# Optimization experiments

Hardware: AMD Instinct MI355X
Metric: run time of the kernel (lower is better)

Reference implementation:

```python
import jax, jax.numpy as jnp
import numpy as np

L = 2
K = 9                      # (L+1)^2 spherical coefficients
N_NODES = 10000
N_EDGES = 80000
C_SPH = 64
C_HID = 64
NHEAD = 8
A_ALPHA = 32
A_VAL = 16
C_OUT = 64
S_GATE = 1 + 2 * L         # gate chunks o_s, o_d^l, o_t^l
EXTRA = NHEAD * A_ALPHA + S_GATE * C_HID   # 256 + 320 = 576

# l-primary -> m-primary permutation for L=2 (m=0 block, then per m: +m coeffs, -m coeffs)
PERM = np.array([0, 2, 6, 3, 7, 1, 5, 8, 4])
INV_PERM = np.argsort(PERM)
L_IDX = np.array([0, 1, 1, 1, 2, 2, 2, 2, 2])  # l of each l-primary coefficient


def scaled_silu(x):
    return jax.nn.silu(x) * (1.0 / 0.6)


def layer_norm(x, w, b, eps=1e-5):
    mu = jnp.mean(x, axis=-1, keepdims=True)
    var = jnp.var(x, axis=-1, keepdims=True)
    return (x - mu) * jax.lax.rsqrt(var + eps) * w + b


def smooth_leaky_relu(x, alpha=0.2):
    return 0.5 * (1 + alpha) * x + 0.5 * (1 - alpha) * x * (2.0 * jax.nn.sigmoid(x) - 1.0)


def _so2_m(x, W):
    # x: [E,2,nin] (row0=+m coeffs, row1=-m coeffs), W: [nin, 2*ncoef*cout]
    y = jnp.einsum('eri,io->ero', x, W)
    half = W.shape[1] // 2
    yr, yi = y[..., :half], y[..., half:]
    out_r = yr[:, 0] - yi[:, 1]
    out_i = yr[:, 1] + yi[:, 0]
    return jnp.stack([out_r, out_i], axis=1)  # [E,2,ncoef*cout]


def so2_conv(emb, cin, cout, wm0, bm0, wm1, wm2, rad=None, extra=0):
    # emb: [E,K,cin] l-primary; block-diagonal per-m SO(2) convolution
    E = emb.shape[0]
    e = emb[:, PERM, :]
    x0 = e[:, 0:3, :].reshape(E, 3 * cin)
    if rad is not None:
        x0 = x0 * rad[:, :3 * cin]
    x0 = x0 @ wm0 + bm0
    x0_extra = None
    if extra:
        x0_extra = x0[:, :extra]
        x0 = x0[:, extra:]
    out0 = x0.reshape(E, 3, cout)
    x1 = e[:, 3:7, :].reshape(E, 2, 2 * cin)
    if rad is not None:
        x1 = x1 * rad[:, 3 * cin:5 * cin][:, None, :]
    out1 = _so2_m(x1, wm1).reshape(E, 4, cout)
    x2 = e[:, 7:9, :].reshape(E, 2, cin)
    if rad is not None:
        x2 = x2 * rad[:, 5 * cin:6 * cin][:, None, :]
    out2 = _so2_m(x2, wm2).reshape(E, 2, cout)
    out = jnp.concatenate([out0, out1, out2], axis=1)[:, INV_PERM, :]
    return out, x0_extra


def _forward(x, atomic_numbers, edge_distance, edge_index, t_ij, rl_ij, wigner, wigner_inv,
             src_emb, tgt_emb, rad_w1, rad_b1, rad_ln_w, rad_ln_b, rad_w2, rad_b2,
             c1_wm0, c1_bm0, c1_wm1, c1_wm2, ln_a_w, ln_a_b, alpha_dot,
             gata_wh, gata_wx, gata_wt, c2_wm0, c2_bm0, c2_wm1, c2_wm2, proj_w, proj_b):
    src, tgt = edge_index[0], edge_index[1]
    x_edge = jnp.concatenate([edge_distance, src_emb[atomic_numbers[src]], tgt_emb[atomic_numbers[tgt]]], axis=1)
    x_src = x[src]                                   # [E,K,C_SPH] gather
    x_tgt = x[tgt]
    h_j = x_tgt[:, 0, :]                              # neighbour scalar part
    X_j = x_tgt[:, 1:, :]                             # neighbour steerable part
    msg = jnp.concatenate([x_src, x_tgt], axis=2)     # [E,K,2*C_SPH]
    msg = jnp.einsum('eij,ejc->eic', wigner, msg)     # per-edge SO(3) rotation
    # radial function: Linear + LayerNorm + ScaledSiLU + Linear
    r = scaled_silu(layer_norm(x_edge @ rad_w1 + rad_b1, rad_ln_w, rad_ln_b)) @ rad_w2 + rad_b2  # [E,768]
    msg, x0_extra = so2_conv(msg, 2 * C_SPH, C_HID, c1_wm0, c1_bm0, c1_wm1, c1_wm2, rad=r, extra=EXTRA)
    a_size = NHEAD * A_ALPHA
    a = x0_extra[:, :a_size].reshape(-1, NHEAD, A_ALPHA)
    attn_out = x0_extra[:, a_size:]                   # [E, S_GATE*C_HID]
    a = smooth_leaky_relu(layer_norm(a, ln_a_w, ln_a_b))
    alpha = jnp.einsum('ehk,hk->eh', a, alpha_dot)    # [E,H]
    # segment softmax over target nodes (torch_geometric.utils.softmax)
    seg_max = jax.ops.segment_max(alpha, tgt, num_segments=N_NODES)
    ex = jnp.exp(alpha - seg_max[tgt])
    denom = jax.ops.segment_sum(ex, tgt, num_segments=N_NODES)
    alpha = ex / (denom[tgt] + 1e-16)
    attn_out = jnp.mean(alpha, axis=1, keepdims=True) * attn_out
    # GATA value activation: gates o_s, o_d^l, o_t^l applied to h_j, X_j, t_ij*rl_ij
    o_s = attn_out[:, :C_HID]
    o_d = attn_out[:, C_HID:(1 + L) * C_HID].reshape(-1, L, C_HID)
    o_t = attn_out[:, (1 + L) * C_HID:].reshape(-1, L, C_HID)
    h = jax.nn.silu(h_j @ gata_wh)                    # [E,C_HID]
    Xp = jnp.einsum('ekc,cd->ekd', X_j, gata_wx)      # [E,K-1,C_HID]
    tp = jax.nn.silu(t_ij @ gata_wt)                  # [E,C_HID]
    parts = [(o_s * h)[:, None, :]]
    for l in range(1, L + 1):
        lo, hi = l * l - 1, (l + 1) * (l + 1) - 1     # rows of this l within X_j / rl_ij
        parts.append(o_d[:, l - 1, None, :] * Xp[:, lo:hi, :]
                     + o_t[:, l - 1, None, :] * (tp[:, None, :] * rl_ij[:, lo:hi, None]))
    msg = jnp.concatenate(parts, axis=1)              # [E,K,C_HID]
    msg, _ = so2_conv(msg, C_HID, NHEAD * A_VAL, c2_wm0, c2_bm0, c2_wm1, c2_wm2)
    E = msg.shape[0]
    msg = (msg.reshape(E, K, NHEAD, A_VAL) * alpha[:, None, :, None]).reshape(E, K, NHEAD * A_VAL)
    msg = jnp.einsum('eij,ejc->eic', wigner_inv, msg)  # rotate back
    node = jax.ops.segment_sum(msg, tgt, num_segments=N_NODES)  # scatter-add to nodes
    out = jnp.einsum('nki,koi->nko', node, proj_w[L_IDX])        # SO3_LinearV2 (per-l weights)
    return out.at[:, 0, :].add(proj_b)


def setup_inputs() -> dict:
    key = jax.random.key(0)
    ks = iter(jax.random.split(key, 48))
    def nrm(shape, scale=1.0):
        return jax.random.normal(next(ks), shape, dtype=jnp.float32) * scale
    inp = {}
    inp['x'] = nrm([N_NODES, K, C_SPH])
    inp['atomic_numbers'] = jax.random.randint(next(ks), (N_NODES,), 0, 100)
    inp['edge_distance'] = nrm([N_EDGES, 64])
    inp['edge_index'] = jax.random.randint(next(ks), (2, N_EDGES), 0, N_NODES)
    inp['t_ij'] = nrm([N_EDGES, 128])
    inp['rl_ij'] = nrm([N_EDGES, K - 1])
    inp['wigner'] = nrm([N_EDGES, K, K], 1.0 / 3.0)
    inp['wigner_inv'] = nrm([N_EDGES, K, K], 1.0 / 3.0)
    inp['src_emb'] = nrm([100, 128], 0.001)
    inp['tgt_emb'] = nrm([100, 128], 0.001)
    inp['rad_w1'] = nrm([320, 128], 320 ** -0.5)
    inp['rad_b1'] = jnp.zeros([128], jnp.float32)
    inp['rad_ln_w'] = jnp.ones([128], jnp.float32)
    inp['rad_ln_b'] = jnp.zeros([128], jnp.float32)
    inp['rad_w2'] = nrm([128, 768], 128 ** -0.5)
    inp['rad_b2'] = jnp.zeros([768], jnp.float32)
    inp['c1_wm0'] = nrm([384, EXTRA + 3 * C_HID], 384 ** -0.5)
    inp['c1_bm0'] = jnp.zeros([EXTRA + 3 * C_HID], jnp.float32)
    inp['c1_wm1'] = nrm([256, 256], 256 ** -0.5)
    inp['c1_wm2'] = nrm([128, 128], 128 ** -0.5)
    inp['ln_a_w'] = jnp.ones([A_ALPHA], jnp.float32)
    inp['ln_a_b'] = jnp.zeros([A_ALPHA], jnp.float32)
    inp['alpha_dot'] = nrm([NHEAD, A_ALPHA], A_ALPHA ** -0.5)
    inp['gata_wh'] = nrm([C_SPH, C_HID], C_SPH ** -0.5)
    inp['gata_wx'] = nrm([C_SPH, C_HID], C_SPH ** -0.5)
    inp['gata_wt'] = nrm([128, C_HID], 128 ** -0.5)
    inp['c2_wm0'] = nrm([3 * C_HID, 3 * NHEAD * A_VAL], (3 * C_HID) ** -0.5)
    inp['c2_bm0'] = jnp.zeros([3 * NHEAD * A_VAL], jnp.float32)
    inp['c2_wm1'] = nrm([2 * C_HID, 2 * NHEAD * A_VAL * 2], (2 * C_HID) ** -0.5)
    inp['c2_wm2'] = nrm([C_HID, 2 * NHEAD * A_VAL], C_HID ** -0.5)
    inp['proj_w'] = nrm([L + 1, C_OUT, NHEAD * A_VAL], (NHEAD * A_VAL) ** -0.5)
    inp['proj_b'] = jnp.zeros([C_OUT], jnp.float32)
    return inp


def reference(x, atomic_numbers, edge_distance, edge_index, t_ij, rl_ij, wigner, wigner_inv,
              src_emb, tgt_emb, rad_w1, rad_b1, rad_ln_w, rad_ln_b, rad_w2, rad_b2,
              c1_wm0, c1_bm0, c1_wm1, c1_wm2, ln_a_w, ln_a_b, alpha_dot,
              gata_wh, gata_wx, gata_wt, c2_wm0, c2_bm0, c2_wm1, c2_wm2, proj_w, proj_b):
    return _forward(x, atomic_numbers, edge_distance, edge_index, t_ij, rl_ij, wigner, wigner_inv,
                    src_emb, tgt_emb, rad_w1, rad_b1, rad_ln_w, rad_ln_b, rad_w2, rad_b2,
                    c1_wm0, c1_bm0, c1_wm1, c1_wm2, ln_a_w, ln_a_b, alpha_dot,
                    gata_wh, gata_wx, gata_wt, c2_wm0, c2_bm0, c2_wm1, c2_wm2, proj_w, proj_b)
```

## Files before the change

kernel.cpp:

```cpp
#include <hip/hip_runtime.h>

#define E_CNT 80000
#define N_NODES 10000

typedef __attribute__((ext_vector_type(8))) __bf16 bf16x8;
typedef __attribute__((ext_vector_type(4))) float f32x4;

__device__ __forceinline__ float sigmoidf_(float x) { return 1.f / (1.f + __expf(-x)); }

__device__ __forceinline__ unsigned fkey(float f) {
  unsigned u = __float_as_uint(f);
  return (u & 0x80000000u) ? ~u : (u | 0x80000000u);
}
__device__ __forceinline__ float unfkey(unsigned k) {
  unsigned u = (k & 0x80000000u) ? (k & 0x7FFFFFFFu) : ~k;
  return __uint_as_float(u);
}

__global__ __launch_bounds__(256) void k_cvt(const float* __restrict__ src,
                                             __bf16* __restrict__ dst,
                                             int K8, int N, int ld) {
  int idx = blockIdx.x * 256 + threadIdx.x;
  if (idx >= K8 * N) return;
  int ksg = idx / N, col = idx % N;
#pragma unroll
  for (int j = 0; j < 8; ++j)
    dst[(size_t)idx * 8 + j] = (__bf16)src[(size_t)(ksg * 8 + j) * ld + col];
}

__global__ __launch_bounds__(256) void k_cvt1(const float* __restrict__ w1,
                                              __bf16* __restrict__ dst) {
  int idx = blockIdx.x * 256 + threadIdx.x;
  if (idx >= 32 * 512) return;
  int ksg = idx >> 9, col = idx & 511;
  int o = col >> 7, c = col & 127;
  const int tc[4] = {0, 128, 256, 384};
  const int bc[4] = {256, 384, 0, 128};
  const float sg[4] = {-1.f, -1.f, 1.f, 1.f};
#pragma unroll
  for (int j = 0; j < 8; ++j) {
    int kk = ksg * 8 + j;
    float v = (kk < 128) ? w1[(size_t)kk * 512 + tc[o] + c]
                         : sg[o] * w1[(size_t)(kk - 128) * 512 + bc[o] + c];
    dst[(size_t)idx * 8 + j] = (__bf16)v;
  }
}

__global__ __launch_bounds__(256) void k_cvt2(const float* __restrict__ w2,
                                              __bf16* __restrict__ dst) {
  int idx = blockIdx.x * 256 + threadIdx.x;
  if (idx >= 16 * 256) return;
  int ksg = idx >> 8, col = idx & 255;
  int o = col >> 7, c = col & 127;
#pragma unroll
  for (int j = 0; j < 8; ++j) {
    int kk = ksg * 8 + j;
    float v;
    if (kk < 64) v = w2[(size_t)kk * 256 + (o == 0 ? c : c + 128)];
    else         v = (o == 0) ? -w2[(size_t)(kk - 64) * 256 + c + 128]
                              :  w2[(size_t)(kk - 64) * 256 + c];
    dst[(size_t)idx * 8 + j] = (__bf16)v;
  }
}

__global__ __launch_bounds__(256, 4) void k_phase1(
    const float* __restrict__ x, const int* __restrict__ an,
    const float* __restrict__ edist, const int* __restrict__ eidx,
    const float* __restrict__ wigner,
    const float* __restrict__ semb, const float* __restrict__ temb,
    const __bf16* __restrict__ rw1f, const float* __restrict__ rb1,
    const float* __restrict__ rlnw, const float* __restrict__ rlnb,
    const __bf16* __restrict__ rw2f, const float* __restrict__ rb2,
    const __bf16* __restrict__ w0r, const float* __restrict__ b0,
    const float* __restrict__ lnaw, const float* __restrict__ lnab,
    const float* __restrict__ adot,
    float* __restrict__ ws_attn, float* __restrict__ ws_apre)
{
  __shared__ __align__(16) float pool[6160];
  __shared__ __align__(16) float bufB[3136];
  __shared__ float wgs[432];
  __shared__ int sidx[16], tidx[16], ansh[16], anth[16];

  const int tid = threadIdx.x;
  const int e0 = blockIdx.x * 16;
  const int lane = tid & 63, wv4 = tid >> 6;
  const int erow = lane & 15, g = lane >> 4;

  __bf16* xe_bf = (__bf16*)pool;
  float* sb = bufB;
  __bf16* sb_bf = (__bf16*)(bufB + 2112);
  __bf16* a_lds2 = (__bf16*)bufB;

  if (tid < 16) {
    int s = eidx[e0 + tid], t = eidx[E_CNT + e0 + tid];
    sidx[tid] = s; tidx[tid] = t; ansh[tid] = an[s]; anth[tid] = an[t];
  }
  for (int i = tid; i < 432; i += 256) {
    int e = i / 27, r = i % 27, kk = r / 9, j = r % 9;
    int row = (kk == 0) ? 0 : (kk == 1 ? 2 : 6);
    wgs[i] = wigner[(size_t)(e0 + e) * 81 + row * 9 + j];
  }
  __syncthreads();

  for (int i = tid; i < 16 * 320; i += 256) {
    int e = i / 320, c = i % 320;
    float v;
    if (c < 64)       v = edist[(size_t)(e0 + e) * 64 + c];
    else if (c < 192) v = semb[ansh[e] * 128 + (c - 64)];
    else              v = temb[anth[e] * 128 + (c - 192)];
    xe_bf[(((c >> 3) * 16 + e) << 3) + (c & 7)] = (__bf16)v;
  }
  __syncthreads();

  {
    bf16x8 af2[10];
#pragma unroll
    for (int ks = 0; ks < 10; ++ks)
      af2[ks] = *(const bf16x8*)(xe_bf + ((ks * 4 + g) * 16 + erow) * 8);
#pragma unroll 1
    for (int tt = 0; tt < 2; ++tt) {
      int col = (wv4 * 2 + tt) * 16 + erow;
      f32x4 acc = {0.f, 0.f, 0.f, 0.f};
#pragma unroll
      for (int ks = 0; ks < 10; ++ks)
        acc = __builtin_amdgcn_mfma_f32_16x16x32_bf16(
            af2[ks], *(const bf16x8*)(rw1f + ((size_t)((ks * 4 + g) * 128) + col) * 8), acc, 0, 0, 0);
      float bb = rb1[col];
#pragma unroll
      for (int r = 0; r < 4; ++r) sb[(g * 4 + r) * 132 + col] = acc[r] + bb;
    }
  }
  __syncthreads();

  {
    int wid = tid >> 6, ln = tid & 63;
    for (int e = wid; e < 16; e += 4) {
      float v0 = sb[e * 132 + ln], v1 = sb[e * 132 + ln + 64];
      float s1 = v0 + v1, s2 = v0 * v0 + v1 * v1;
#pragma unroll
      for (int m = 32; m >= 1; m >>= 1) {
        s1 += __shfl_xor(s1, m);
        s2 += __shfl_xor(s2, m);
      }
      float mu = s1 * (1.f / 128.f);
      float var = s2 * (1.f / 128.f) - mu * mu;
      float rstd = rsqrtf(var + 1e-5f);
      float y0 = (v0 - mu) * rstd * rlnw[ln] + rlnb[ln];
      float y1 = (v1 - mu) * rstd * rlnw[ln + 64] + rlnb[ln + 64];
      sb[e * 132 + ln]      = y0 * sigmoidf_(y0) * (1.f / 0.6f);
      sb[e * 132 + ln + 64] = y1 * sigmoidf_(y1) * (1.f / 0.6f);
    }
  }
  __syncthreads();

  {
    int ksg = tid >> 4, e = tid & 15;
    const float* sp = sb + e * 132 + ksg * 8;
    float4 u0 = *(const float4*)sp;
    float4 u1 = *(const float4*)(sp + 4);
    bf16x8 v;
    v[0] = (__bf16)u0.x; v[1] = (__bf16)u0.y; v[2] = (__bf16)u0.z; v[3] = (__bf16)u0.w;
    v[4] = (__bf16)u1.x; v[5] = (__bf16)u1.y; v[6] = (__bf16)u1.z; v[7] = (__bf16)u1.w;
    *(bf16x8*)(sb_bf + (ksg * 16 + e) * 8) = v;
  }
  __syncthreads();

  float* rbuf = pool;
  {
    bf16x8 af3[4];
#pragma unroll
    for (int ks = 0; ks < 4; ++ks)
      af3[ks] = *(const bf16x8*)(sb_bf + ((ks * 4 + g) * 16 + erow) * 8);
#pragma unroll 1
    for (int tt = 0; tt < 6; ++tt) {
      int col = (wv4 * 6 + tt) * 16 + erow;
      f32x4 acc = {0.f, 0.f, 0.f, 0.f};
#pragma unroll
      for (int ks = 0; ks < 4; ++ks)
        acc = __builtin_amdgcn_mfma_f32_16x16x32_bf16(
            af3[ks], *(const bf16x8*)(rw2f + ((size_t)((ks * 4 + g) * 384) + col) * 8), acc, 0, 0, 0);
      float bb = rb2[col];
#pragma unroll
      for (int r = 0; r < 4; ++r) rbuf[(g * 4 + r) * 385 + col] = acc[r] + bb;
    }
  }
  __syncthreads();

  {
    int e = tid & 15, cg = tid >> 4;
    int c0 = cg * 8;
    const float* xb = (c0 < 64) ? (x + (size_t)sidx[e] * 576 + c0)
                                : (x + (size_t)tidx[e] * 576 + (c0 - 64));
    float xc[9][8];
#pragma unroll
    for (int j = 0; j < 9; ++j) {
      float4 u0 = *(const float4*)(xb + j * 64);
      float4 u1 = *(const float4*)(xb + j * 64 + 4);
      xc[j][0] = u0.x; xc[j][1] = u0.y; xc[j][2] = u0.z; xc[j][3] = u0.w;
      xc[j][4] = u1.x; xc[j][5] = u1.y; xc[j][6] = u1.z; xc[j][7] = u1.w;
    }
#pragma unroll
    for (int kk = 0; kk < 3; ++kk) {
      float wv[9];
#pragma unroll
      for (int j = 0; j < 9; ++j) wv[j] = wgs[e * 27 + kk * 9 + j];
      __bf16* ap = a_lds2 + ((kk * 16 + cg) * 16 + e) * 8;
#pragma unroll
      for (int cu = 0; cu < 8; ++cu) {
        float m = 0.f;
#pragma unroll
        for (int j = 0; j < 9; ++j) m += wv[j] * xc[j][cu];
        int colc = kk * 128 + c0 + cu;
        ap[cu] = (__bf16)(m * rbuf[e * 385 + colc]);
      }
    }
  }
  __syncthreads();

  float* sb5 = pool;
  {
    bf16x8 af[12];
#pragma unroll
    for (int ks = 0; ks < 12; ++ks)
      af[ks] = *(const bf16x8*)(a_lds2 + ((ks * 4 + g) * 16 + erow) * 8);
#pragma unroll 1
    for (int tt = 0; tt < 9; ++tt) {
      int tile = wv4 * 9 + tt;
      int col = tile * 16 + erow;
      f32x4 acc = {0.f, 0.f, 0.f, 0.f};
#pragma unroll
      for (int ks = 0; ks < 12; ++ks) {
        bf16x8 bf = *(const bf16x8*)(w0r + ((size_t)((ks * 4 + g) * 576) + col) * 8);
        acc = __builtin_amdgcn_mfma_f32_16x16x32_bf16(af[ks], bf, acc, 0, 0, 0);
      }
      if (tile < 16) {
#pragma unroll
        for (int r = 0; r < 4; ++r) sb5[(g * 4 + r) * 260 + col] = acc[r];
      } else {
        float bb = b0[col];
#pragma unroll
        for (int r = 0; r < 4; ++r)
          ws_attn[(size_t)(e0 + g * 4 + r) * 320 + (col - 256)] = acc[r] + bb;
      }
    }
  }
  __syncthreads();

  {
    float bb = b0[tid];
    int h = tid >> 5, kk = tid & 31;
    float lw = lnaw[kk], lb = lnab[kk], ad = adot[h * 32 + kk];
#pragma unroll
    for (int e = 0; e < 16; ++e) {
      float v = sb5[e * 260 + tid] + bb;
      float s1 = v, s2 = v * v;
#pragma unroll
      for (int m = 16; m >= 1; m >>= 1) {
        s1 += __shfl_xor(s1, m);
        s2 += __shfl_xor(s2, m);
      }
      float mu = s1 * (1.f / 32.f);
      float var = s2 * (1.f / 32.f) - mu * mu;
      float rstd = rsqrtf(var + 1e-5f);
      float xn = (v - mu) * rstd * lw + lb;
      float sl = 0.6f * xn + 0.4f * xn * (2.f * sigmoidf_(xn) - 1.f);
      float p = sl * ad;
#pragma unroll
      for (int m = 16; m >= 1; m >>= 1) p += __shfl_xor(p, m);
      if (kk == 0) ws_apre[(size_t)(e0 + e) * 8 + h] = p;
    }
  }
}

__global__ __launch_bounds__(256) void k_segmax(const float* __restrict__ apre,
                                                const int* __restrict__ eidx,
                                                unsigned* __restrict__ segk) {
  int idx = blockIdx.x * 256 + threadIdx.x;
  if (idx >= E_CNT * 8) return;
  int e = idx >> 3, h = idx & 7;
  int t = eidx[E_CNT + e];
  atomicMax(&segk[t * 8 + h], fkey(apre[idx]));
}

__global__ __launch_bounds__(256) void k_expsum(const float* __restrict__ apre,
                                                const int* __restrict__ eidx,
                                                const unsigned* __restrict__ segk,
                                                float* __restrict__ ex_out,
                                                float* __restrict__ denom) {
  int idx = blockIdx.x * 256 + threadIdx.x;
  if (idx >= E_CNT * 8) return;
  int e = idx >> 3, h = idx & 7;
  int t = eidx[E_CNT + e];
  float m = unfkey(segk[t * 8 + h]);
  float ex = __expf(apre[idx] - m);
  ex_out[idx] = ex;
  atomicAdd(&denom[t * 8 + h], ex);
}

__global__ __launch_bounds__(256, 3) void k_phase2(
    const float* __restrict__ x, const int* __restrict__ eidx,
    const float* __restrict__ t_ij, const float* __restrict__ rl_ij,
    const float* __restrict__ winv,
    const __bf16* __restrict__ gwhf, const __bf16* __restrict__ gwxf, const __bf16* __restrict__ gwtf,
    const __bf16* __restrict__ w0b, const float* __restrict__ b0,
    const __bf16* __restrict__ w1n, const __bf16* __restrict__ w2n,
    const float* __restrict__ ws_attn, const float* __restrict__ ws_ex,
    const float* __restrict__ denom,
    float* __restrict__ node)
{
  __shared__ __align__(16) __bf16 mb[9 * 8 * 16 * 8];
  __shared__ __align__(16) __bf16 tbf[16 * 16 * 8];
  __shared__ float wib[16 * 81];
  __shared__ float alp[128];
  __shared__ float rlb[128];
  __shared__ float malp[16];
  __shared__ int tnode[16];

  const int tid = threadIdx.x;
  const int e0 = blockIdx.x * 16;
  const int lane = tid & 63, wv = tid >> 6;
  const int e16 = lane & 15, g = lane >> 4;

  if (tid < 16) tnode[tid] = eidx[E_CNT + e0 + tid];
  __syncthreads();

  if (tid < 128) {
    int e = tid >> 3, h = tid & 7;
    float ex = ws_ex[(size_t)(e0 + e) * 8 + h];
    alp[tid] = ex / (denom[tnode[e] * 8 + h] + 1e-16f);
  } else {
    int i = tid - 128;
    rlb[i] = rl_ij[(size_t)(e0 + (i >> 3)) * 8 + (i & 7)];
  }
  for (int i = tid; i < 16 * 81; i += 256)
    wib[i] = winv[(size_t)(e0 + i / 81) * 81 + i % 81];

  for (int i = tid; i < 1152; i += 256) {
    int e = i / 72, rk = i % 72;
    const float* sp = x + (size_t)tnode[e] * 576 + rk * 8;
    float4 u0 = *(const float4*)sp;
    float4 u1 = *(const float4*)(sp + 4);
    bf16x8 v;
    v[0] = (__bf16)u0.x; v[1] = (__bf16)u0.y; v[2] = (__bf16)u0.z; v[3] = (__bf16)u0.w;
    v[4] = (__bf16)u1.x; v[5] = (__bf16)u1.y; v[6] = (__bf16)u1.z; v[7] = (__bf16)u1.w;
    *(bf16x8*)(mb + ((size_t)rk * 16 + e) * 8) = v;
  }
  {
    int e = tid >> 4, ksg = tid & 15;
    const float* sp = t_ij + (size_t)(e0 + e) * 128 + ksg * 8;
    float4 u0 = *(const float4*)sp;
    float4 u1 = *(const float4*)(sp + 4);
    bf16x8 v;
    v[0] = (__bf16)u0.x; v[1] = (__bf16)u0.y; v[2] = (__bf16)u0.z; v[3] = (__bf16)u0.w;
    v[4] = (__bf16)u1.x; v[5] = (__bf16)u1.y; v[6] = (__bf16)u1.z; v[7] = (__bf16)u1.w;
    *(bf16x8*)(tbf + ((size_t)ksg * 16 + e) * 8) = v;
  }
  __syncthreads();
  if (tid < 16) {
    float s = 0.f;
#pragma unroll
    for (int h = 0; h < 8; ++h) s += alp[tid * 8 + h];
    malp[tid] = s * 0.125f;
  }
  __syncthreads();

  f32x4 M0, M1, M2, M3, M4, M5, M6, M7, M8;
  {
    const int c = wv * 16 + e16;
#define MF(a, b, acc) acc = __builtin_amdgcn_mfma_f32_16x16x32_bf16(a, b, acc, 0, 0, 0)
#define MBF(row, ksg) (*(const bf16x8*)(mb + (((row) * 8 + (ksg)) * 16 + e16) * 8))
    f32x4 tv4;
    {
      f32x4 acc = {0.f, 0.f, 0.f, 0.f};
#pragma unroll
      for (int ks = 0; ks < 4; ++ks)
        MF(*(const bf16x8*)(tbf + ((ks * 4 + g) * 16 + e16) * 8),
           *(const bf16x8*)(gwtf + ((size_t)((ks * 4 + g) * 64) + c) * 8), acc);
#pragma unroll
      for (int r = 0; r < 4; ++r) { float v = acc[r]; tv4[r] = v * sigmoidf_(v); }
    }
    f32x4 hv4;
    {
      f32x4 acc = {0.f, 0.f, 0.f, 0.f};
      MF(MBF(0, g), *(const bf16x8*)(gwhf + ((size_t)(g * 64) + c) * 8), acc);
      MF(MBF(0, 4 + g), *(const bf16x8*)(gwhf + ((size_t)((4 + g) * 64) + c) * 8), acc);
#pragma unroll
      for (int r = 0; r < 4; ++r) { float v = acc[r]; hv4[r] = v * sigmoidf_(v); }
    }
    f32x4 osv, od0v, od1v, ot0v, ot1v;
#pragma unroll
    for (int r = 0; r < 4; ++r) {
      int e = g * 4 + r;
      float ml = malp[e];
      const float* wsb = ws_attn + (size_t)(e0 + e) * 320;
      osv[r]  = wsb[c] * ml;
      od0v[r] = wsb[64 + c] * ml;
      od1v[r] = wsb[128 + c] * ml;
      ot0v[r] = wsb[192 + c] * ml;
      ot1v[r] = wsb[256 + c] * ml;
    }
#pragma unroll
    for (int r = 0; r < 4; ++r) M0[r] = osv[r] * hv4[r];
    bf16x8 bx0 = *(const bf16x8*)(gwxf + ((size_t)(g * 64) + c) * 8);
    bf16x8 bx1 = *(const bf16x8*)(gwxf + ((size_t)((4 + g) * 64) + c) * 8);
#define XROW(rr, MV, odv, otv, jj)                                        \
    {                                                                     \
      f32x4 acc = {0.f, 0.f, 0.f, 0.f};                                   \
      MF(MBF(rr, g), bx0, acc);                                           \
      MF(MBF(rr, 4 + g), bx1, acc);                                       \
      _Pragma("unroll")                                                   \
      for (int r = 0; r < 4; ++r) {                                       \
        int e = g * 4 + r;                                                \
        MV[r] = odv[r] * acc[r] + otv[r] * tv4[r] * rlb[e * 8 + (jj)];    \
      }                                                                   \
    }
    XROW(1, M1, od0v, ot0v, 0)
    XROW(2, M2, od0v, ot0v, 1)
    XROW(3, M3, od0v, ot0v, 2)
    XROW(4, M4, od1v, ot1v, 3)
    XROW(5, M5, od1v, ot1v, 4)
    XROW(6, M6, od1v, ot1v, 5)
    XROW(7, M7, od1v, ot1v, 6)
    XROW(8, M8, od1v, ot1v, 7)
#undef XROW
#undef MBF
  }
  __syncthreads();

  {
    const int c = wv * 16 + e16;
    const int cksg = c >> 3, cj = c & 7;
#define WOUT(rr, MV)                                                       \
    {                                                                      \
      _Pragma("unroll")                                                    \
      for (int r = 0; r < 4; ++r) {                                        \
        int e = g * 4 + r;                                                 \
        mb[(((rr) * 8 + cksg) * 16 + e) * 8 + cj] = (__bf16)MV[r];         \
      }                                                                    \
    }
    WOUT(0, M0) WOUT(1, M1) WOUT(2, M2) WOUT(3, M3) WOUT(4, M4)
    WOUT(5, M5) WOUT(6, M6) WOUT(7, M7) WOUT(8, M8)
#undef WOUT
  }
  __syncthreads();

  {
#define AF(row, ks) (*(const bf16x8*)(mb + (((row) * 8 + (ks)) * 16 + e16) * 8))
#define MF2(a, b, acc) acc = __builtin_amdgcn_mfma_f32_16x16x32_bf16(a, b, acc, 0, 0, 0)
#pragma unroll 1
    for (int gi = 0; gi < 2; ++gi) {
      const int c = (wv * 2 + gi) * 16 + e16;
      const int h = c >> 4;
      const float av0 = alp[(g * 4 + 0) * 8 + h];
      const float av1 = alp[(g * 4 + 1) * 8 + h];
      const float av2 = alp[(g * 4 + 2) * 8 + h];
      const float av3 = alp[(g * 4 + 3) * 8 + h];
      const float* wp0 = wib + (g * 4 + 0) * 81;
      const float* wp1 = wib + (g * 4 + 1) * 81;
      const float* wp2 = wib + (g * 4 + 2) * 81;
      const float* wp3 = wib + (g * 4 + 3) * 81;
      f32x4 oa[9];
#pragma unroll
      for (int i = 0; i < 9; ++i) oa[i] = (f32x4){0.f, 0.f, 0.f, 0.f};

      {
        bf16x8 a0 = AF(0, g), a1 = AF(0, 4 + g);
        bf16x8 a2 = AF(2, g), a3 = AF(2, 4 + g);
        bf16x8 a4 = AF(6, g), a5 = AF(6, 4 + g);
#pragma unroll 1
        for (int o = 0; o < 3; ++o) {
          const __bf16* wp = w0b + ((size_t)(g * 384) + o * 128 + c) * 8;
          f32x4 acc = {0.f, 0.f, 0.f, 0.f};
          MF2(a0, *(const bf16x8*)(wp + (size_t)0 * 4 * 384 * 8), acc);
          MF2(a1, *(const bf16x8*)(wp + (size_t)1 * 4 * 384 * 8), acc);
          MF2(a2, *(const bf16x8*)(wp + (size_t)2 * 4 * 384 * 8), acc);
          MF2(a3, *(const bf16x8*)(wp + (size_t)3 * 4 * 384 * 8), acc);
          MF2(a4, *(const bf16x8*)(wp + (size_t)4 * 4 * 384 * 8), acc);
          MF2(a5, *(const bf16x8*)(wp + (size_t)5 * 4 * 384 * 8), acc);
          const int j = (o == 0) ? 0 : (o == 1) ? 2 : 6;
          const float bb = b0[o * 128 + c];
          const float t0 = (acc[0] + bb) * av0;
          const float t1 = (acc[1] + bb) * av1;
          const float t2 = (acc[2] + bb) * av2;
          const float t3 = (acc[3] + bb) * av3;
#pragma unroll
          for (int i = 0; i < 9; ++i) {
            oa[i][0] += wp0[i * 9 + j] * t0;
            oa[i][1] += wp1[i * 9 + j] * t1;
            oa[i][2] += wp2[i * 9 + j] * t2;
            oa[i][3] += wp3[i * 9 + j] * t3;
          }
        }
      }
      {
        bf16x8 a0 = AF(3, g), a1 = AF(3, 4 + g);
        bf16x8 a2 = AF(7, g), a3 = AF(7, 4 + g);
        bf16x8 a4 = AF(1, g), a5 = AF(1, 4 + g);
        bf16x8 a6 = AF(5, g), a7 = AF(5, 4 + g);
#pragma unroll 1
        for (int o = 0; o < 4; ++o) {
          const __bf16* wp = w1n + ((size_t)(g * 512) + o * 128 + c) * 8;
          f32x4 acc = {0.f, 0.f, 0.f, 0.f};
          MF2(a0, *(const bf16x8*)(wp + (size_t)0 * 4 * 512 * 8), acc);
          MF2(a1, *(const bf16x8*)(wp + (size_t)1 * 4 * 512 * 8), acc);
          MF2(a2, *(const bf16x8*)(wp + (size_t)2 * 4 * 512 * 8), acc);
          MF2(a3, *(const bf16x8*)(wp + (size_t)3 * 4 * 512 * 8), acc);
          MF2(a4, *(const bf16x8*)(wp + (size_t)4 * 4 * 512 * 8), acc);
          MF2(a5, *(const bf16x8*)(wp + (size_t)5 * 4 * 512 * 8), acc);
          MF2(a6, *(const bf16x8*)(wp + (size_t)6 * 4 * 512 * 8), acc);
          MF2(a7, *(const bf16x8*)(wp + (size_t)7 * 4 * 512 * 8), acc);
          const int j = (o == 0) ? 3 : (o == 1) ? 7 : (o == 2) ? 1 : 5;
          const float t0 = acc[0] * av0;
          const float t1 = acc[1] * av1;
          const float t2 = acc[2] * av2;
          const float t3 = acc[3] * av3;
#pragma unroll
          for (int i = 0; i < 9; ++i) {
            oa[i][0] += wp0[i * 9 + j] * t0;
            oa[i][1] += wp1[i * 9 + j] * t1;
            oa[i][2] += wp2[i * 9 + j] * t2;
            oa[i][3] += wp3[i * 9 + j] * t3;
          }
        }
      }
      {
        bf16x8 a0 = AF(8, g), a1 = AF(8, 4 + g);
        bf16x8 a2 = AF(4, g), a3 = AF(4, 4 + g);
#pragma unroll 1
        for (int o = 0; o < 2; ++o) {
          const __bf16* wp = w2n + ((size_t)(g * 256) + o * 128 + c) * 8;
          f32x4 acc = {0.f, 0.f, 0.f, 0.f};
          MF2(a0, *(const bf16x8*)(wp + (size_t)0 * 4 * 256 * 8), acc);
          MF2(a1, *(const bf16x8*)(wp + (size_t)1 * 4 * 256 * 8), acc);
          MF2(a2, *(const bf16x8*)(wp + (size_t)2 * 4 * 256 * 8), acc);
          MF2(a3, *(const bf16x8*)(wp + (size_t)3 * 4 * 256 * 8), acc);
          const int j = (o == 0) ? 8 : 4;
          const float t0 = acc[0] * av0;
          const float t1 = acc[1] * av1;
          const float t2 = acc[2] * av2;
          const float t3 = acc[3] * av3;
#pragma unroll
          for (int i = 0; i < 9; ++i) {
            oa[i][0] += wp0[i * 9 + j] * t0;
            oa[i][1] += wp1[i * 9 + j] * t1;
            oa[i][2] += wp2[i * 9 + j] * t2;
            oa[i][3] += wp3[i * 9 + j] * t3;
          }
        }
      }
#pragma unroll
      for (int r = 0; r < 4; ++r) {
        float* np = node + (size_t)tnode[g * 4 + r] * 1152 + c;
#pragma unroll
        for (int i = 0; i < 9; ++i) atomicAdd(np + i * 128, oa[i][r]);
      }
    }
#undef MF2
#undef AF
#undef MF
  }
}

__global__ __launch_bounds__(256) void k_wt(const float* __restrict__ pw, float* __restrict__ wT) {
  int idx = blockIdx.x * 256 + threadIdx.x;
  if (idx >= 3 * 128 * 64) return;
  int l = idx / 8192, r = idx % 8192, i = r / 64, o = r % 64;
  wT[idx] = pw[(l * 64 + o) * 128 + i];
}

__global__ __launch_bounds__(256) void k_proj(const float* __restrict__ node,
                                              const float* __restrict__ wT,
                                              const float* __restrict__ pb,
                                              float* __restrict__ out) {
  __shared__ __align__(16) float A[32 * 132];
  int k = blockIdx.y;
  int n0 = blockIdx.x * 32;
  const int lidx = (k == 0) ? 0 : (k <= 3 ? 1 : 2);
  int tid = threadIdx.x;
  for (int i = tid; i < 32 * 128; i += 256) {
    int nn = i >> 7, ii = i & 127;
    int n = n0 + nn;
    A[nn * 132 + ii] = (n < N_NODES) ? node[((size_t)n * 9 + k) * 128 + ii] : 0.f;
  }
  __syncthreads();
  int o = tid & 63, wid = tid >> 6;
  float acc[8] = {0.f, 0.f, 0.f, 0.f, 0.f, 0.f, 0.f, 0.f};
#pragma unroll 4
  for (int i = 0; i < 128; ++i) {
    float w = wT[lidx * 8192 + i * 64 + o];
#pragma unroll
    for (int r = 0; r < 8; ++r) acc[r] += A[(wid * 8 + r) * 132 + i] * w;
  }
  float bias = (k == 0) ? pb[o] : 0.f;
#pragma unroll
  for (int r = 0; r < 8; ++r) {
    int n = n0 + wid * 8 + r;
    if (n < N_NODES) out[((size_t)n * 9 + k) * 64 + o] = acc[r] + bias;
  }
}

extern "C" void kernel_launch(void* const* d_in, const int* in_sizes, int n_in,
                              void* d_out, int out_size, void* d_ws, size_t ws_size,
                              hipStream_t stream) {
  const float* x      = (const float*)d_in[0];
  const int*   an     = (const int*)d_in[1];
  const float* edist  = (const float*)d_in[2];
  const int*   eidx   = (const int*)d_in[3];
  const float* t_ij   = (const float*)d_in[4];
  const float* rl_ij  = (const float*)d_in[5];
  const float* wig    = (const float*)d_in[6];
  const float* winv   = (const float*)d_in[7];
  const float* semb   = (const float*)d_in[8];
  const float* temb   = (const float*)d_in[9];
  const float* rw1    = (const float*)d_in[10];
  const float* rb1    = (const float*)d_in[11];
  const float* rlnw   = (const float*)d_in[12];
  const float* rlnb   = (const float*)d_in[13];
  const float* rw2    = (const float*)d_in[14];
  const float* rb2    = (const float*)d_in[15];
  const float* c1w0   = (const float*)d_in[16];
  const float* c1b0   = (const float*)d_in[17];
  const float* lnaw   = (const float*)d_in[20];
  const float* lnab   = (const float*)d_in[21];
  const float* adot   = (const float*)d_in[22];
  const float* gwh    = (const float*)d_in[23];
  const float* gwx    = (const float*)d_in[24];
  const float* gwt    = (const float*)d_in[25];
  const float* c2w0   = (const float*)d_in[26];
  const float* c2b0   = (const float*)d_in[27];
  const float* c2w1   = (const float*)d_in[28];
  const float* c2w2   = (const float*)d_in[29];
  const float* pw     = (const float*)d_in[30];
  const float* pb     = (const float*)d_in[31];
  float* out = (float*)d_out;

  char* p = (char*)d_ws;
  float* ws_attn  = (float*)p; p += (size_t)E_CNT * 320 * 4;
  float* ws_apre  = (float*)p; p += (size_t)E_CNT * 8 * 4;
  float* ws_ex    = (float*)p; p += (size_t)E_CNT * 8 * 4;
  unsigned* segk  = (unsigned*)p; p += (size_t)N_NODES * 8 * 4;
  float* denom    = (float*)p; p += (size_t)N_NODES * 8 * 4;
  float* node     = (float*)p; p += (size_t)N_NODES * 1152 * 4;
  float* wT       = (float*)p; p += (size_t)3 * 128 * 64 * 4;
  __bf16* w0r     = (__bf16*)p; p += (size_t)48 * 576 * 8 * 2;
  __bf16* w0b     = (__bf16*)p; p += (size_t)24 * 384 * 8 * 2;
  __bf16* w1n     = (__bf16*)p; p += (size_t)32 * 512 * 8 * 2;
  __bf16* w2n     = (__bf16*)p; p += (size_t)16 * 256 * 8 * 2;
  __bf16* rw1f    = (__bf16*)p; p += (size_t)40 * 128 * 8 * 2;
  __bf16* rw2f    = (__bf16*)p; p += (size_t)16 * 384 * 8 * 2;
  __bf16* gwhf    = (__bf16*)p; p += (size_t)8 * 64 * 8 * 2;
  __bf16* gwxf    = (__bf16*)p; p += (size_t)8 * 64 * 8 * 2;
  __bf16* gwtf    = (__bf16*)p; p += (size_t)16 * 64 * 8 * 2;

  hipMemsetAsync(segk, 0, N_NODES * 8 * 4, stream);
  hipMemsetAsync(denom, 0, N_NODES * 8 * 4, stream);
  hipMemsetAsync(node, 0, (size_t)N_NODES * 1152 * 4, stream);

  k_cvt<<<108, 256, 0, stream>>>(c1w0, w0r, 48, 576, 768);
  k_cvt<<<36, 256, 0, stream>>>(c2w0, w0b, 24, 384, 384);
  k_cvt1<<<64, 256, 0, stream>>>(c2w1, w1n);
  k_cvt2<<<16, 256, 0, stream>>>(c2w2, w2n);
  k_cvt<<<20, 256, 0, stream>>>(rw1, rw1f, 40, 128, 128);
  k_cvt<<<24, 256, 0, stream>>>(rw2, rw2f, 16, 384, 768);
  k_cvt<<<2, 256, 0, stream>>>(gwh, gwhf, 8, 64, 64);
  k_cvt<<<2, 256, 0, stream>>>(gwx, gwxf, 8, 64, 64);
  k_cvt<<<4, 256, 0, stream>>>(gwt, gwtf, 16, 64, 64);
  k_wt<<<96, 256, 0, stream>>>(pw, wT);
  k_phase1<<<E_CNT / 16, 256, 0, stream>>>(x, an, edist, eidx, wig, semb, temb,
                                           rw1f, rb1, rlnw, rlnb, rw2f, rb2,
                                           w0r, c1b0, lnaw, lnab, adot,
                                           ws_attn, ws_apre);
  k_segmax<<<(E_CNT * 8) / 256, 256, 0, stream>>>(ws_apre, eidx, segk);
  k_expsum<<<(E_CNT * 8) / 256, 256, 0, stream>>>(ws_apre, eidx, segk, ws_ex, denom);
  k_phase2<<<E_CNT / 16, 256, 0, stream>>>(x, eidx, t_ij, rl_ij, winv,
                                           gwhf, gwxf, gwtf, w0b, c2b0, w1n, w2n,
                                           ws_attn, ws_ex, denom, node);
  k_proj<<<dim3((N_NODES + 31) / 32, 9), 256, 0, stream>>>(node, wT, pb, out);
}
```

Measured before the change: 786.5 us.

## Merge weight-prep launches, fuse segment max into phase1, split MFMA accumulators

Ten weight-conversion and transpose kernels become a single k_prep launch, cutting per-launch overhead. The segment-max atomicMax is folded into k_phase1's attention-logit epilogue, which removes the separate k_segmax kernel and its re-read of the logits. MFMA accumulation chains in k_phase2 are split into two interleaved accumulators to shorten the dependent MFMA latency chain, at the cost of extra registers and a final add.

```diff
diff --git a/kernel.cpp b/kernel.cpp
--- a/kernel.cpp
+++ b/kernel.cpp
@@ -17,49 +17,90 @@
   return __uint_as_float(u);
 }
 
-__global__ __launch_bounds__(256) void k_cvt(const float* __restrict__ src,
-                                             __bf16* __restrict__ dst,
-                                             int K8, int N, int ld) {
-  int idx = blockIdx.x * 256 + threadIdx.x;
-  if (idx >= K8 * N) return;
-  int ksg = idx / N, col = idx % N;
-#pragma unroll
-  for (int j = 0; j < 8; ++j)
-    dst[(size_t)idx * 8 + j] = (__bf16)src[(size_t)(ksg * 8 + j) * ld + col];
-}
-
-__global__ __launch_bounds__(256) void k_cvt1(const float* __restrict__ w1,
-                                              __bf16* __restrict__ dst) {
-  int idx = blockIdx.x * 256 + threadIdx.x;
-  if (idx >= 32 * 512) return;
-  int ksg = idx >> 9, col = idx & 511;
-  int o = col >> 7, c = col & 127;
-  const int tc[4] = {0, 128, 256, 384};
-  const int bc[4] = {256, 384, 0, 128};
-  const float sg[4] = {-1.f, -1.f, 1.f, 1.f};
-#pragma unroll
-  for (int j = 0; j < 8; ++j) {
-    int kk = ksg * 8 + j;
-    float v = (kk < 128) ? w1[(size_t)kk * 512 + tc[o] + c]
-                         : sg[o] * w1[(size_t)(kk - 128) * 512 + bc[o] + c];
-    dst[(size_t)idx * 8 + j] = (__bf16)v;
-  }
-}
-
-__global__ __launch_bounds__(256) void k_cvt2(const float* __restrict__ w2,
-                                              __bf16* __restrict__ dst) {
-  int idx = blockIdx.x * 256 + threadIdx.x;
-  if (idx >= 16 * 256) return;
-  int ksg = idx >> 8, col = idx & 255;
-  int o = col >> 7, c = col & 127;
-#pragma unroll
-  for (int j = 0; j < 8; ++j) {
-    int kk = ksg * 8 + j;
-    float v;
-    if (kk < 64) v = w2[(size_t)kk * 256 + (o == 0 ? c : c + 128)];
-    else         v = (o == 0) ? -w2[(size_t)(kk - 64) * 256 + c + 128]
-                              :  w2[(size_t)(kk - 64) * 256 + c];
-    dst[(size_t)idx * 8 + j] = (__bf16)v;
+__global__ __launch_bounds__(256) void k_prep(
+    const float* __restrict__ c1w0, const float* __restrict__ c2w0,
+    const float* __restrict__ c2w1, const float* __restrict__ c2w2,
+    const float* __restrict__ rw1, const float* __restrict__ rw2,
+    const float* __restrict__ gwh, const float* __restrict__ gwx,
+    const float* __restrict__ gwt, const float* __restrict__ pw,
+    __bf16* __restrict__ w0r, __bf16* __restrict__ w0b,
+    __bf16* __restrict__ w1n, __bf16* __restrict__ w2n,
+    __bf16* __restrict__ rw1f, __bf16* __restrict__ rw2f,
+    __bf16* __restrict__ gwhf, __bf16* __restrict__ gwxf,
+    __bf16* __restrict__ gwtf, float* __restrict__ wT) {
+  int i = blockIdx.x * 256 + threadIdx.x;
+  if (i < 27648) {
+    int ksg = i / 576, col = i % 576;
+#pragma unroll
+    for (int j = 0; j < 8; ++j)
+      w0r[(size_t)i * 8 + j] = (__bf16)c1w0[(size_t)(ksg * 8 + j) * 768 + col];
+  } else if (i < 36864) {
+    int ii = i - 27648;
+    int ksg = ii / 384, col = ii % 384;
+#pragma unroll
+    for (int j = 0; j < 8; ++j)
+      w0b[(size_t)ii * 8 + j] = (__bf16)c2w0[(size_t)(ksg * 8 + j) * 384 + col];
+  } else if (i < 53248) {
+    int ii = i - 36864;
+    int ksg = ii >> 9, col = ii & 511;
+    int o = col >> 7, c = col & 127;
+    const int tc[4] = {0, 128, 256, 384};
+    const int bc[4] = {256, 384, 0, 128};
+    const float sg[4] = {-1.f, -1.f, 1.f, 1.f};
+#pragma unroll
+    for (int j = 0; j < 8; ++j) {
+      int kk = ksg * 8 + j;
+      float v = (kk < 128) ? c2w1[(size_t)kk * 512 + tc[o] + c]
+                           : sg[o] * c2w1[(size_t)(kk - 128) * 512 + bc[o] + c];
+      w1n[(size_t)ii * 8 + j] = (__bf16)v;
+    }
+  } else if (i < 57344) {
+    int ii = i - 53248;
+    int ksg = ii >> 8, col = ii & 255;
+    int o = col >> 7, c = col & 127;
+#pragma unroll
+    for (int j = 0; j < 8; ++j) {
+      int kk = ksg * 8 + j;
+      float v;
+      if (kk < 64) v = c2w2[(size_t)kk * 256 + (o == 0 ? c : c + 128)];
+      else         v = (o == 0) ? -c2w2[(size_t)(kk - 64) * 256 + c + 128]
+                                :  c2w2[(size_t)(kk - 64) * 256 + c];
+      w2n[(size_t)ii * 8 + j] = (__bf16)v;
+    }
+  } else if (i < 62464) {
+    int ii = i - 57344;
+    int ksg = ii / 128, col = ii % 128;
+#pragma unroll
+    for (int j = 0; j < 8; ++j)
+      rw1f[(size_t)ii * 8 + j] = (__bf16)rw1[(size_t)(ksg * 8 + j) * 128 + col];
+  } else if (i < 68608) {
+    int ii = i - 62464;
+    int ksg = ii / 384, col = ii % 384;
+#pragma unroll
+    for (int j = 0; j < 8; ++j)
+      rw2f[(size_t)ii * 8 + j] = (__bf16)rw2[(size_t)(ksg * 8 + j) * 768 + col];
+  } else if (i < 69120) {
+    int ii = i - 68608;
+    int ksg = ii / 64, col = ii % 64;
+#pragma unroll
+    for (int j = 0; j < 8; ++j)
+      gwhf[(size_t)ii * 8 + j] = (__bf16)gwh[(size_t)(ksg * 8 + j) * 64 + col];
+  } else if (i < 69632) {
+    int ii = i - 69120;
+    int ksg = ii / 64, col = ii % 64;
+#pragma unroll
+    for (int j = 0; j < 8; ++j)
+      gwxf[(size_t)ii * 8 + j] = (__bf16)gwx[(size_t)(ksg * 8 + j) * 64 + col];
+  } else if (i < 70656) {
+    int ii = i - 69632;
+    int ksg = ii / 64, col = ii % 64;
+#pragma unroll
+    for (int j = 0; j < 8; ++j)
+      gwtf[(size_t)ii * 8 + j] = (__bf16)gwt[(size_t)(ksg * 8 + j) * 64 + col];
+  } else if (i < 95232) {
+    int ii = i - 70656;
+    int l = ii / 8192, r = ii % 8192, ir = r / 64, o = r % 64;
+    wT[ii] = pw[(size_t)(l * 64 + o) * 128 + ir];
   }
 }
 
@@ -74,7 +115,8 @@
     const __bf16* __restrict__ w0r, const float* __restrict__ b0,
     const float* __restrict__ lnaw, const float* __restrict__ lnab,
     const float* __restrict__ adot,
-    float* __restrict__ ws_attn, float* __restrict__ ws_apre)
+    float* __restrict__ ws_attn, float* __restrict__ ws_apre,
+    unsigned* __restrict__ segk)
 {
   __shared__ __align__(16) float pool[6160];
   __shared__ __align__(16) float bufB[3136];
@@ -267,19 +309,12 @@
       float p = sl * ad;
 #pragma unroll
       for (int m = 16; m >= 1; m >>= 1) p += __shfl_xor(p, m);
-      if (kk == 0) ws_apre[(size_t)(e0 + e) * 8 + h] = p;
-    }
-  }
-}
-
-__global__ __launch_bounds__(256) void k_segmax(const float* __restrict__ apre,
-                                                const int* __restrict__ eidx,
-                                                unsigned* __restrict__ segk) {
-  int idx = blockIdx.x * 256 + threadIdx.x;
-  if (idx >= E_CNT * 8) return;
-  int e = idx >> 3, h = idx & 7;
-  int t = eidx[E_CNT + e];
-  atomicMax(&segk[t * 8 + h], fkey(apre[idx]));
+      if (kk == 0) {
+        ws_apre[(size_t)(e0 + e) * 8 + h] = p;
+        atomicMax(&segk[tidx[e] * 8 + h], fkey(p));
+      }
+    }
+  }
 }
 
 __global__ __launch_bounds__(256) void k_expsum(const float* __restrict__ apre,
@@ -371,21 +406,25 @@
 #define MBF(row, ksg) (*(const bf16x8*)(mb + (((row) * 8 + (ksg)) * 16 + e16) * 8))
     f32x4 tv4;
     {
-      f32x4 acc = {0.f, 0.f, 0.f, 0.f};
-#pragma unroll
-      for (int ks = 0; ks < 4; ++ks)
-        MF(*(const bf16x8*)(tbf + ((ks * 4 + g) * 16 + e16) * 8),
-           *(const bf16x8*)(gwtf + ((size_t)((ks * 4 + g) * 64) + c) * 8), acc);
-#pragma unroll
-      for (int r = 0; r < 4; ++r) { float v = acc[r]; tv4[r] = v * sigmoidf_(v); }
+      f32x4 aA = {0.f, 0.f, 0.f, 0.f}, aB = {0.f, 0.f, 0.f, 0.f};
+      MF(*(const bf16x8*)(tbf + ((0 * 4 + g) * 16 + e16) * 8),
+         *(const bf16x8*)(gwtf + ((size_t)((0 * 4 + g) * 64) + c) * 8), aA);
+      MF(*(const bf16x8*)(tbf + ((1 * 4 + g) * 16 + e16) * 8),
+         *(const bf16x8*)(gwtf + ((size_t)((1 * 4 + g) * 64) + c) * 8), aB);
+      MF(*(const bf16x8*)(tbf + ((2 * 4 + g) * 16 + e16) * 8),
+         *(const bf16x8*)(gwtf + ((size_t)((2 * 4 + g) * 64) + c) * 8), aA);
+      MF(*(const bf16x8*)(tbf + ((3 * 4 + g) * 16 + e16) * 8),
+         *(const bf16x8*)(gwtf + ((size_t)((3 * 4 + g) * 64) + c) * 8), aB);
+#pragma unroll
+      for (int r = 0; r < 4; ++r) { float v = aA[r] + aB[r]; tv4[r] = v * sigmoidf_(v); }
     }
     f32x4 hv4;
     {
-      f32x4 acc = {0.f, 0.f, 0.f, 0.f};
-      MF(MBF(0, g), *(const bf16x8*)(gwhf + ((size_t)(g * 64) + c) * 8), acc);
-      MF(MBF(0, 4 + g), *(const bf16x8*)(gwhf + ((size_t)((4 + g) * 64) + c) * 8), acc);
-#pragma unroll
-      for (int r = 0; r < 4; ++r) { float v = acc[r]; hv4[r] = v * sigmoidf_(v); }
+      f32x4 aA = {0.f, 0.f, 0.f, 0.f}, aB = {0.f, 0.f, 0.f, 0.f};
+      MF(MBF(0, g), *(const bf16x8*)(gwhf + ((size_t)(g * 64) + c) * 8), aA);
+      MF(MBF(0, 4 + g), *(const bf16x8*)(gwhf + ((size_t)((4 + g) * 64) + c) * 8), aB);
+#pragma unroll
+      for (int r = 0; r < 4; ++r) { float v = aA[r] + aB[r]; hv4[r] = v * sigmoidf_(v); }
     }
     f32x4 osv, od0v, od1v, ot0v, ot1v;
 #pragma unroll
@@ -405,13 +444,13 @@
     bf16x8 bx1 = *(const bf16x8*)(gwxf + ((size_t)((4 + g) * 64) + c) * 8);
 #define XROW(rr, MV, odv, otv, jj)                                        \
     {                                                                     \
-      f32x4 acc = {0.f, 0.f, 0.f, 0.f};                                   \
-      MF(MBF(rr, g), bx0, acc);                                           \
-      MF(MBF(rr, 4 + g), bx1, acc);                                       \
+      f32x4 aA = {0.f, 0.f, 0.f, 0.f}, aB = {0.f, 0.f, 0.f, 0.f};         \
+      MF(MBF(rr, g), bx0, aA);                                            \
+      MF(MBF(rr, 4 + g), bx1, aB);                                        \
       _Pragma("unroll")                                                   \
       for (int r = 0; r < 4; ++r) {                                       \
         int e = g * 4 + r;                                                \
-        MV[r] = odv[r] * acc[r] + otv[r] * tv4[r] * rlb[e * 8 + (jj)];    \
+        MV[r] = odv[r] * (aA[r] + aB[r]) + otv[r] * tv4[r] * rlb[e * 8 + (jj)]; \
       }                                                                   \
     }
     XROW(1, M1, od0v, ot0v, 0)
@@ -470,19 +509,19 @@
 #pragma unroll 1
         for (int o = 0; o < 3; ++o) {
           const __bf16* wp = w0b + ((size_t)(g * 384) + o * 128 + c) * 8;
-          f32x4 acc = {0.f, 0.f, 0.f, 0.f};
-          MF2(a0, *(const bf16x8*)(wp + (size_t)0 * 4 * 384 * 8), acc);
-          MF2(a1, *(const bf16x8*)(wp + (size_t)1 * 4 * 384 * 8), acc);
-          MF2(a2, *(const bf16x8*)(wp + (size_t)2 * 4 * 384 * 8), acc);
-          MF2(a3, *(const bf16x8*)(wp + (size_t)3 * 4 * 384 * 8), acc);
-          MF2(a4, *(const bf16x8*)(wp + (size_t)4 * 4 * 384 * 8), acc);
-          MF2(a5, *(const bf16x8*)(wp + (size_t)5 * 4 * 384 * 8), acc);
+          f32x4 aA = {0.f, 0.f, 0.f, 0.f}, aB = {0.f, 0.f, 0.f, 0.f};
+          MF2(a0, *(const bf16x8*)(wp + (size_t)0 * 4 * 384 * 8), aA);
+          MF2(a1, *(const bf16x8*)(wp + (size_t)1 * 4 * 384 * 8), aB);
+          MF2(a2, *(const bf16x8*)(wp + (size_t)2 * 4 * 384 * 8), aA);
+          MF2(a3, *(const bf16x8*)(wp + (size_t)3 * 4 * 384 * 8), aB);
+          MF2(a4, *(const bf16x8*)(wp + (size_t)4 * 4 * 384 * 8), aA);
+          MF2(a5, *(const bf16x8*)(wp + (size_t)5 * 4 * 384 * 8), aB);
           const int j = (o == 0) ? 0 : (o == 1) ? 2 : 6;
           const float bb = b0[o * 128 + c];
-          const float t0 = (acc[0] + bb) * av0;
-          const float t1 = (acc[1] + bb) * av1;
-          const float t2 = (acc[2] + bb) * av2;
-          const float t3 = (acc[3] + bb) * av3;
+          const float t0 = (aA[0] + aB[0] + bb) * av0;
+          const float t1 = (aA[1] + aB[1] + bb) * av1;
+          const float t2 = (aA[2] + aB[2] + bb) * av2;
+          const float t3 = (aA[3] + aB[3] + bb) * av3;
 #pragma unroll
           for (int i = 0; i < 9; ++i) {
             oa[i][0] += wp0[i * 9 + j] * t0;
@@ -500,20 +539,20 @@
 #pragma unroll 1
         for (int o = 0; o < 4; ++o) {
           const __bf16* wp = w1n + ((size_t)(g * 512) + o * 128 + c) * 8;
-          f32x4 acc = {0.f, 0.f, 0.f, 0.f};
-          MF2(a0, *(const bf16x8*)(wp + (size_t)0 * 4 * 512 * 8), acc);
-          MF2(a1, *(const bf16x8*)(wp + (size_t)1 * 4 * 512 * 8), acc);
-          MF2(a2, *(const bf16x8*)(wp + (size_t)2 * 4 * 512 * 8), acc);
-          MF2(a3, *(const bf16x8*)(wp + (size_t)3 * 4 * 512 * 8), acc);
-          MF2(a4, *(const bf16x8*)(wp + (size_t)4 * 4 * 512 * 8), acc);
-          MF2(a5, *(const bf16x8*)(wp + (size_t)5 * 4 * 512 * 8), acc);
-          MF2(a6, *(const bf16x8*)(wp + (size_t)6 * 4 * 512 * 8), acc);
-          MF2(a7, *(const bf16x8*)(wp + (size_t)7 * 4 * 512 * 8), acc);
+          f32x4 aA = {0.f, 0.f, 0.f, 0.f}, aB = {0.f, 0.f, 0.f, 0.f};
+          MF2(a0, *(const bf16x8*)(wp + (size_t)0 * 4 * 512 * 8), aA);
+          MF2(a1, *(const bf16x8*)(wp + (size_t)1 * 4 * 512 * 8), aB);
+          MF2(a2, *(const bf16x8*)(wp + (size_t)2 * 4 * 512 * 8), aA);
+          MF2(a3, *(const bf16x8*)(wp + (size_t)3 * 4 * 512 * 8), aB);
+          MF2(a4, *(const bf16x8*)(wp + (size_t)4 * 4 * 512 * 8), aA);
+          MF2(a5, *(const bf16x8*)(wp + (size_t)5 * 4 * 512 * 8), aB);
+          MF2(a6, *(const bf16x8*)(wp + (size_t)6 * 4 * 512 * 8), aA);
+          MF2(a7, *(const bf16x8*)(wp + (size_t)7 * 4 * 512 * 8), aB);
           const int j = (o == 0) ? 3 : (o == 1) ? 7 : (o == 2) ? 1 : 5;
-          const float t0 = acc[0] * av0;
-          const float t1 = acc[1] * av1;
-          const float t2 = acc[2] * av2;
-          const float t3 = acc[3] * av3;
+          const float t0 = (aA[0] + aB[0]) * av0;
+          const float t1 = (aA[1] + aB[1]) * av1;
+          const float t2 = (aA[2] + aB[2]) * av2;
+          const float t3 = (aA[3] + aB[3]) * av3;
 #pragma unroll
           for (int i = 0; i < 9; ++i) {
             oa[i][0] += wp0[i * 9 + j] * t0;
@@ -529,16 +568,16 @@
 #pragma unroll 1
         for (int o = 0; o < 2; ++o) {
           const __bf16* wp = w2n + ((size_t)(g * 256) + o * 128 + c) * 8;
-          f32x4 acc = {0.f, 0.f, 0.f, 0.f};
-          MF2(a0, *(const bf16x8*)(wp + (size_t)0 * 4 * 256 * 8), acc);
-          MF2(a1, *(const bf16x8*)(wp + (size_t)1 * 4 * 256 * 8), acc);
-          MF2(a2, *(const bf16x8*)(wp + (size_t)2 * 4 * 256 * 8), acc);
-          MF2(a3, *(const bf16x8*)(wp + (size_t)3 * 4 * 256 * 8), acc);
+          f32x4 aA = {0.f, 0.f, 0.f, 0.f}, aB = {0.f, 0.f, 0.f, 0.f};
+          MF2(a0, *(const bf16x8*)(wp + (size_t)0 * 4 * 256 * 8), aA);
+          MF2(a1, *(const bf16x8*)(wp + (size_t)1 * 4 * 256 * 8), aB);
+          MF2(a2, *(const bf16x8*)(wp + (size_t)2 * 4 * 256 * 8), aA);
+          MF2(a3, *(const bf16x8*)(wp + (size_t)3 * 4 * 256 * 8), aB);
           const int j = (o == 0) ? 8 : 4;
-          const float t0 = acc[0] * av0;
-          const float t1 = acc[1] * av1;
-          const float t2 = acc[2] * av2;
-          const float t3 = acc[3] * av3;
+          const float t0 = (aA[0] + aB[0]) * av0;
+          const float t1 = (aA[1] + aB[1]) * av1;
+          const float t2 = (aA[2] + aB[2]) * av2;
+          const float t3 = (aA[3] + aB[3]) * av3;
 #pragma unroll
           for (int i = 0; i < 9; ++i) {
             oa[i][0] += wp0[i * 9 + j] * t0;
@@ -559,13 +598,6 @@
 #undef AF
 #undef MF
   }
-}
-
-__global__ __launch_bounds__(256) void k_wt(const float* __restrict__ pw, float* __restrict__ wT) {
-  int idx = blockIdx.x * 256 + threadIdx.x;
-  if (idx >= 3 * 128 * 64) return;
-  int l = idx / 8192, r = idx % 8192, i = r / 64, o = r % 64;
-  wT[idx] = pw[(l * 64 + o) * 128 + i];
 }
 
 __global__ __launch_bounds__(256) void k_proj(const float* __restrict__ node,
@@ -656,21 +688,12 @@
   hipMemsetAsync(denom, 0, N_NODES * 8 * 4, stream);
   hipMemsetAsync(node, 0, (size_t)N_NODES * 1152 * 4, stream);
 
-  k_cvt<<<108, 256, 0, stream>>>(c1w0, w0r, 48, 576, 768);
-  k_cvt<<<36, 256, 0, stream>>>(c2w0, w0b, 24, 384, 384);
-  k_cvt1<<<64, 256, 0, stream>>>(c2w1, w1n);
-  k_cvt2<<<16, 256, 0, stream>>>(c2w2, w2n);
-  k_cvt<<<20, 256, 0, stream>>>(rw1, rw1f, 40, 128, 128);
-  k_cvt<<<24, 256, 0, stream>>>(rw2, rw2f, 16, 384, 768);
-  k_cvt<<<2, 256, 0, stream>>>(gwh, gwhf, 8, 64, 64);
-  k_cvt<<<2, 256, 0, stream>>>(gwx, gwxf, 8, 64, 64);
-  k_cvt<<<4, 256, 0, stream>>>(gwt, gwtf, 16, 64, 64);
-  k_wt<<<96, 256, 0, stream>>>(pw, wT);
+  k_prep<<<372, 256, 0, stream>>>(c1w0, c2w0, c2w1, c2w2, rw1, rw2, gwh, gwx, gwt, pw,
+                                  w0r, w0b, w1n, w2n, rw1f, rw2f, gwhf, gwxf, gwtf, wT);
   k_phase1<<<E_CNT / 16, 256, 0, stream>>>(x, an, edist, eidx, wig, semb, temb,
                                            rw1f, rb1, rlnw, rlnb, rw2f, rb2,
                                            w0r, c1b0, lnaw, lnab, adot,
-                                           ws_attn, ws_apre);
-  k_segmax<<<(E_CNT * 8) / 256, 256, 0, stream>>>(ws_apre, eidx, segk);
+                                           ws_attn, ws_apre, segk);
   k_expsum<<<(E_CNT * 8) / 256, 256, 0, stream>>>(ws_apre, eidx, segk, ws_ex, denom);
   k_phase2<<<E_CNT / 16, 256, 0, stream>>>(x, eidx, t_ij, rl_ij, winv,
                                            gwhf, gwxf, gwtf, w0b, c2b0, w1n, w2n,
```

New measurement: 786.7 us. Within noise of the previous version (+0.0%).
